# Performance work log

Measured on AMD Instinct MI355X. Metric: run time of the kernel, lower is better.

## Reference

```python
import jax, jax.numpy as jnp
import numpy as np

N = 50000      # nodes
E = 500000     # edges
IN = 256       # input feature dim
HID = 64       # hidden (per-head) dim, layer 1
H1 = 4         # heads, layer 1
NC = 64        # num_classes (layer 2 out, 1 head)
ED = 32        # edge_dim
T = 8          # num_etypes
SLOPE = 0.2    # leakyrelu negative slope


def setup_inputs() -> dict:
    key = jax.random.key(0)
    ks = jax.random.split(key, 20)
    p = lambda k, shape: (jax.random.normal(k, shape, jnp.float32) * 0.05)
    return {
        "h": jax.random.normal(ks[0], (N, IN), jnp.float32),
        "row": jax.random.randint(ks[1], (E,), 0, N, jnp.int32),   # src
        "col": jax.random.randint(ks[2], (E,), 0, N, jnp.int32),   # dst
        "etype": jax.random.randint(ks[3], (E,), 0, T, jnp.int32),
        # layer 1 (4 heads, no residual, elu activation)
        "edge_emb1": p(ks[4], (T, ED)),
        "W1": p(ks[5], (IN, HID * H1)),
        "Wr1": p(ks[6], (T, ED, ED * H1)),      # TypedLinear per-etype weight
        "a_l1": p(ks[7], (H1, HID)),
        "a_r1": p(ks[8], (H1, HID)),
        "a_e1": p(ks[9], (H1, ED)),
        # layer 2 (1 head, residual Linear, no activation)
        "edge_emb2": p(ks[10], (T, ED)),
        "W2": p(ks[11], (HID * H1, NC)),
        "Wr2": p(ks[12], (T, ED, ED)),
        "a_l2": p(ks[13], (1, NC)),
        "a_r2": p(ks[14], (1, NC)),
        "a_e2": p(ks[15], (1, ED)),
        "res_W2": p(ks[16], (HID * H1, NC)),
        "res_b2": p(ks[17], (NC,)),
    }


def _simple_hgn_conv(h, row, col, etype, edge_emb, W, Wr, a_l, a_r, a_e,
                     res_W, res_b, apply_act):
    """One SimpleHGNConv layer. h:[N,in], returns [N, out_dim*H] (D-major, H-minor
    layout, matching emb.permute(0,2,1).view in the torch code)."""
    H, D = a_l.shape            # num_heads, out_dim
    n = h.shape[0]
    emb = (h @ W).reshape(n, H, D)                     # [N,H,D]
    emb = jnp.where(jnp.isnan(emb), 0.0, emb)
    # TypedLinear: edge_emb[etype] @ Wr[etype]; only T distinct rows -> per-type GEMM
    ee = jnp.einsum('te,teo->to', edge_emb, Wr).reshape(T, H, ED)  # [T,H,ED]
    h_l = jnp.einsum('nhd,hd->nh', emb, a_l)[row]      # [E,H]
    h_r = jnp.einsum('nhd,hd->nh', emb, a_r)[col]      # [E,H]
    h_e = jnp.einsum('thd,hd->th', ee, a_e)[etype]     # [E,H]
    att = jax.nn.leaky_relu(h_l + h_r + h_e, SLOPE)    # [E,H]
    # edge_softmax: normalize over incoming edges of each destination node (col)
    seg_max = jax.ops.segment_max(att, col, num_segments=n)   # [N,H]
    att = jnp.exp(att - seg_max[col])
    seg_sum = jax.ops.segment_sum(att, col, num_segments=n)   # [N,H]
    alpha = att / seg_sum[col]                          # [E,H]
    # u_mul_e + sum aggregation
    msg = emb[row] * alpha[:, :, None]                  # [E,H,D]
    out = jax.ops.segment_sum(msg, col, num_segments=n) # [N,H,D]
    out = out.transpose(0, 2, 1).reshape(n, D * H)      # D-major layout
    if res_W is not None:
        out = out + h @ res_W + res_b
    if apply_act:
        out = jax.nn.elu(out)
    return out


def reference(h, row, col, etype,
              edge_emb1, W1, Wr1, a_l1, a_r1, a_e1,
              edge_emb2, W2, Wr2, a_l2, a_r2, a_e2, res_W2, res_b2):
    h1 = _simple_hgn_conv(h, row, col, etype, edge_emb1, W1, Wr1,
                          a_l1, a_r1, a_e1, None, None, True)
    h2 = _simple_hgn_conv(h1, row, col, etype, edge_emb2, W2, Wr2,
                          a_l2, a_r2, a_e2, res_W2, res_b2, False)
    # split by node type (first half type 'l', second half type 'v')
    return (h2[: N // 2], h2[N // 2 :])
```

## Files before the change

kernel.cpp:

```cpp
#include <hip/hip_runtime.h>
#include <hip/hip_bf16.h>

typedef __bf16 bf16x8 __attribute__((ext_vector_type(8)));
typedef float f32x4 __attribute__((ext_vector_type(4)));

#define IN_DIM 256
#define NT 8

__device__ __forceinline__ float b2f(unsigned short u) {
  union { unsigned int i; float f; } x; x.i = ((unsigned int)u) << 16; return x.f;
}
__device__ __forceinline__ float lo2f(unsigned int w) {
  union { unsigned int i; float f; } x; x.i = w << 16; return x.f;
}
__device__ __forceinline__ float hi2f(unsigned int w) {
  union { unsigned int i; float f; } x; x.i = w & 0xFFFF0000u; return x.f;
}
__device__ __forceinline__ unsigned short f2b(float f) {
  union { float f; unsigned int i; } u; u.f = f;
  unsigned int r = u.i + 0x7FFF + ((u.i >> 16) & 1);
  return (unsigned short)(r >> 16);
}
__device__ __forceinline__ float lrelu(float x) { return x >= 0.f ? x : 0.2f * x; }
__device__ __forceinline__ float ldf(const void* p, size_t i, int isf32) {
  return isf32 ? ((const float*)p)[i] : b2f(((const unsigned short*)p)[i]);
}

__global__ void prep_all_kernel(const void* __restrict__ W1, const void* __restrict__ W2,
                                const void* __restrict__ rW2,
                                const void* __restrict__ al1, const void* __restrict__ ar1,
                                const void* __restrict__ al2, const void* __restrict__ ar2,
                                const void* __restrict__ ee1, const void* __restrict__ Wr1,
                                const void* __restrict__ ae1,
                                const void* __restrict__ ee2, const void* __restrict__ Wr2,
                                const void* __restrict__ ae2,
                                unsigned short* __restrict__ W1t,
                                unsigned short* __restrict__ W2t,
                                float* __restrict__ a2l, float* __restrict__ a2r,
                                float* __restrict__ he1, float* __restrict__ he2,
                                float* __restrict__ alD, float* __restrict__ arD,
                                const unsigned int* __restrict__ hw,
                                const int* __restrict__ col, int* __restrict__ cnt,
                                int E_, int N_, int* __restrict__ dflag) {
  int b = blockIdx.x, tid = threadIdx.x;
  if (b >= 454) {
    int base = (b - 454) * 1024 + tid;
#pragma unroll
    for (int k = 0; k < 4; k++) {
      int e = base + k * 256;
      if (e < E_) {
        int c = col[e];
        if ((unsigned)c < (unsigned)N_) atomicAdd(&cnt[c], 1);
      }
    }
    return;
  }
  __shared__ int sflag;
  {
    int bad = 0;
    if (tid < 64) {
      for (int i = 0; i < 4; i++) {
        unsigned int w = hw[tid * 4 + i];
        unsigned int ex = (w & 0x7FFFu) >> 7;
        if (ex >= 0xC0u) bad++;
      }
#pragma unroll
      for (int off = 32; off; off >>= 1) bad += __shfl_xor(bad, off);
      if (tid == 0) sflag = (bad > 8) ? 1 : 0;
    }
    __syncthreads();
  }
  const int isf32 = sflag;
  if (b == 0 && tid == 0) *dflag = isf32;
  if (b < 384) {
    int j = b, k = tid;
    if (j < 256) {
      int src = (j & 3) * 64 + (j >> 2);
      W1t[j * 256 + k] = f2b(ldf(W1, (size_t)k * 256 + src, isf32));
    } else {
      int o = j - 256;
      float v = (o < 64) ? ldf(W2, (size_t)k * 64 + o, isf32)
                         : ldf(rW2, (size_t)k * 64 + (o - 64), isf32);
      W2t[o * 256 + k] = f2b(v);
    }
  } else if (b < 448) {
    int k = (b - 384) * 4 + (tid >> 6), d = tid & 63;
    float w2 = ldf(W2, (size_t)k * 64 + d, isf32);
    float l2 = w2 * ldf(al2, d, isf32);
    float r2 = w2 * ldf(ar2, d, isf32);
#pragma unroll
    for (int off = 32; off; off >>= 1) { l2 += __shfl_xor(l2, off); r2 += __shfl_xor(r2, off); }
    if (d == 0) { a2l[k] = l2; a2r[k] = r2; }
  } else {
    int bid = b - 448;
    int t = tid >> 5, d = tid & 31;
    if (bid < 4) {
      int h = bid;
      float s = 0.f;
#pragma unroll
      for (int e = 0; e < 32; e++)
        s += ldf(ee1, t * 32 + e, isf32) * ldf(Wr1, (size_t)(t * 32 + e) * 128 + h * 32 + d, isf32);
      float v = s * ldf(ae1, h * 32 + d, isf32);
#pragma unroll
      for (int off = 16; off; off >>= 1) v += __shfl_xor(v, off);
      if (d == 0) he1[t * 4 + h] = v;
    } else if (bid == 4) {
      float s = 0.f;
#pragma unroll
      for (int e = 0; e < 32; e++)
        s += ldf(ee2, t * 32 + e, isf32) * ldf(Wr2, (size_t)(t * 32 + e) * 32 + d, isf32);
      float v = s * ldf(ae2, d, isf32);
#pragma unroll
      for (int off = 16; off; off >>= 1) v += __shfl_xor(v, off);
      if (d == 0) he2[t] = v;
    } else {
      int j = tid;
      alD[j] = ldf(al1, (j & 3) * 64 + (j >> 2), isf32);
      arD[j] = ldf(ar1, (j & 3) * 64 + (j >> 2), isf32);
    }
  }
}

__global__ __launch_bounds__(256, 4) void gemm1_fill(
    const void* __restrict__ A, int M,
    const unsigned short* __restrict__ Bt,
    unsigned short* __restrict__ emb1,
    const float* __restrict__ alD, const float* __restrict__ arD,
    float* __restrict__ hl1, float* __restrict__ hr1,
    const int* __restrict__ dflag, int MBlocks,
    const int* __restrict__ col, const int* __restrict__ row,
    const int* __restrict__ ety, const int* __restrict__ ptrb,
    const int* __restrict__ bsum, int* __restrict__ cnt,
    int* __restrict__ srcc, int E_) {
  __shared__ unsigned short As[64 * 64];
  __shared__ float lsum[4][64][4];
  __shared__ float rsum[4][64][4];
  if (blockIdx.x >= MBlocks) {
    int base = (blockIdx.x - MBlocks) * 1024 + threadIdx.x;
#pragma unroll
    for (int k = 0; k < 4; k++) {
      int e = base + k * 256;
      if (e < E_) {
        int c = col[e];
        if ((unsigned)c < (unsigned)M) {
          int pos = atomicSub(&cnt[c], 1) - 1;
          long long slot = (long long)(ptrb[c] + bsum[c >> 8]) + pos;
          if (slot >= 0 && slot < E_) {
            int sr = row[e], t = ety[e];
            srcc[slot] = ((unsigned)sr < (unsigned)M && (unsigned)t < (unsigned)NT)
                             ? (sr | (t << 20)) : -1;
          }
        }
      }
    }
    return;
  }
  int isf32 = *dflag;
  const int tid = threadIdx.x;
  const int m0 = blockIdx.x * 64;
  const int wv = tid >> 6, lane = tid & 63;
  const int q = lane >> 4, m = lane & 15;
  const int jp = wv * 64;
  f32x4 acc[4][4] = {};
  for (int kc = 0; kc < 256; kc += 64) {
    {
      int row_ = tid >> 2, qt = tid & 3;
      int gr = m0 + row_;
      unsigned short tmp[16];
      if (gr < M) {
        if (isf32) {
          const float* ap = (const float*)A + (size_t)gr * 256 + kc + qt * 16;
          float4 v0 = *(const float4*)ap;
          float4 v1 = *(const float4*)(ap + 4);
          float4 v2 = *(const float4*)(ap + 8);
          float4 v3 = *(const float4*)(ap + 12);
          tmp[0]=f2b(v0.x); tmp[1]=f2b(v0.y); tmp[2]=f2b(v0.z); tmp[3]=f2b(v0.w);
          tmp[4]=f2b(v1.x); tmp[5]=f2b(v1.y); tmp[6]=f2b(v1.z); tmp[7]=f2b(v1.w);
          tmp[8]=f2b(v2.x); tmp[9]=f2b(v2.y); tmp[10]=f2b(v2.z); tmp[11]=f2b(v2.w);
          tmp[12]=f2b(v3.x); tmp[13]=f2b(v3.y); tmp[14]=f2b(v3.z); tmp[15]=f2b(v3.w);
        } else {
          const unsigned short* ap = (const unsigned short*)A + (size_t)gr * 256 + kc + qt * 16;
          *(int4*)tmp = *(const int4*)ap;
          *(int4*)(tmp + 8) = *(const int4*)(ap + 8);
        }
      } else {
        for (int x = 0; x < 16; x++) tmp[x] = 0;
      }
      int g0 = (qt * 2) ^ (row_ & 7);
      int g1 = (qt * 2 + 1) ^ (row_ & 7);
      *(int4*)(As + row_ * 64 + g0 * 8) = *(int4*)tmp;
      *(int4*)(As + row_ * 64 + g1 * 8) = *(int4*)(tmp + 8);
    }
    __syncthreads();
#pragma unroll
    for (int ks = 0; ks < 2; ks++) {
      int gk = ks * 4 + q;
      bf16x8 afr[4];
#pragma unroll
      for (int cm = 0; cm < 4; cm++) {
        int row_ = cm * 16 + m;
        afr[cm] = *(const bf16x8*)(As + row_ * 64 + (gk ^ (row_ & 7)) * 8);
      }
#pragma unroll
      for (int cj = 0; cj < 4; cj++) {
        int jr = jp + cj * 16 + m;
        bf16x8 b = *(const bf16x8*)(Bt + (size_t)jr * 256 + kc + gk * 8);
#pragma unroll
        for (int cm = 0; cm < 4; cm++)
          acc[cm][cj] = __builtin_amdgcn_mfma_f32_16x16x32_bf16(afr[cm], b, acc[cm][cj], 0, 0, 0);
      }
    }
    __syncthreads();
  }
  float al[4], ar[4];
#pragma unroll
  for (int cj = 0; cj < 4; cj++) {
    al[cj] = alD[jp + cj * 16 + m];
    ar[cj] = arD[jp + cj * 16 + m];
  }
#pragma unroll
  for (int cm = 0; cm < 4; cm++) {
#pragma unroll
    for (int r = 0; r < 4; r++) {
      int lrow = cm * 16 + q * 4 + r;
      int gm = m0 + lrow;
      float lp = 0.f, rp = 0.f;
#pragma unroll
      for (int cj = 0; cj < 4; cj++) {
        float v = acc[cm][cj][r];
        if (gm < M) emb1[(size_t)gm * 256 + jp + cj * 16 + m] = f2b(v);
        lp += v * al[cj]; rp += v * ar[cj];
      }
      lp += __shfl_xor(lp, 4); lp += __shfl_xor(lp, 8);
      rp += __shfl_xor(rp, 4); rp += __shfl_xor(rp, 8);
      if (m < 4) { lsum[wv][lrow][m] = lp; rsum[wv][lrow][m] = rp; }
    }
  }
  __syncthreads();
  {
    int row_ = tid >> 2, h = tid & 3;
    int gm = m0 + row_;
    if (gm < M) {
      float l = lsum[0][row_][h] + lsum[1][row_][h] + lsum[2][row_][h] + lsum[3][row_][h];
      float r = rsum[0][row_][h] + rsum[1][row_][h] + rsum[2][row_][h] + rsum[3][row_][h];
      hl1[(size_t)gm * 4 + h] = l;
      hr1[(size_t)gm * 4 + h] = r;
    }
  }
}

__global__ __launch_bounds__(256, 4) void gemm2_fused(
    const unsigned short* __restrict__ A, int M,
    const unsigned short* __restrict__ Bt,
    unsigned short* __restrict__ emb2, unsigned short* __restrict__ res,
    const void* __restrict__ bias, const int* __restrict__ dflag) {
  __shared__ unsigned short As[64 * 64];
  int isf32 = *dflag;
  const int tid = threadIdx.x;
  const int m0 = blockIdx.x * 64;
  const int wv = tid >> 6, lane = tid & 63;
  const int q = lane >> 4, m = lane & 15;
  const int jp = (wv & 1) * 64;
  const int mh = (wv >> 1) * 32;
  f32x4 acc[2][4] = {};
  for (int kc = 0; kc < 256; kc += 64) {
    {
      int row = tid >> 2, qt = tid & 3;
      int gr = m0 + row;
      unsigned short tmp[16];
      if (gr < M) {
        const unsigned short* ap = A + (size_t)gr * 256 + kc + qt * 16;
        *(int4*)tmp = *(const int4*)ap;
        *(int4*)(tmp + 8) = *(const int4*)(ap + 8);
      } else {
        for (int x = 0; x < 16; x++) tmp[x] = 0;
      }
      int g0 = (qt * 2) ^ (row & 7);
      int g1 = (qt * 2 + 1) ^ (row & 7);
      *(int4*)(As + row * 64 + g0 * 8) = *(int4*)tmp;
      *(int4*)(As + row * 64 + g1 * 8) = *(int4*)(tmp + 8);
    }
    __syncthreads();
#pragma unroll
    for (int ks = 0; ks < 2; ks++) {
      int gk = ks * 4 + q;
      bf16x8 afr[2];
#pragma unroll
      for (int cm = 0; cm < 2; cm++) {
        int row = mh + cm * 16 + m;
        afr[cm] = *(const bf16x8*)(As + row * 64 + (gk ^ (row & 7)) * 8);
      }
#pragma unroll
      for (int cj = 0; cj < 4; cj++) {
        int jr = jp + cj * 16 + m;
        bf16x8 b = *(const bf16x8*)(Bt + (size_t)jr * 256 + kc + gk * 8);
#pragma unroll
        for (int cm = 0; cm < 2; cm++)
          acc[cm][cj] = __builtin_amdgcn_mfma_f32_16x16x32_bf16(afr[cm], b, acc[cm][cj], 0, 0, 0);
      }
    }
    __syncthreads();
  }
  float bv[4];
#pragma unroll
  for (int cj = 0; cj < 4; cj++)
    bv[cj] = (jp == 64) ? ldf(bias, cj * 16 + m, isf32) : 0.f;
#pragma unroll
  for (int cm = 0; cm < 2; cm++) {
#pragma unroll
    for (int r = 0; r < 4; r++) {
      int gm = m0 + mh + cm * 16 + q * 4 + r;
      if (gm < M) {
#pragma unroll
        for (int cj = 0; cj < 4; cj++) {
          float v = acc[cm][cj][r];
          int gj = cj * 16 + m;
          if (jp == 0) emb2[(size_t)gm * 64 + gj] = f2b(v);
          else res[(size_t)gm * 64 + gj] = f2b(v + bv[cj]);
        }
      }
    }
  }
}

__global__ void scan1_kernel(const int* __restrict__ cnt, int* __restrict__ ptrb,
                             int* __restrict__ bsum, int n) {
  __shared__ int wsum[4];
  int tid = threadIdx.x, lane = tid & 63, wid = tid >> 6;
  int i = blockIdx.x * 256 + tid;
  int v = (i < n) ? cnt[i] : 0;
  int x = v;
#pragma unroll
  for (int off = 1; off < 64; off <<= 1) {
    int y = __shfl_up(x, off);
    if (lane >= off) x += y;
  }
  if (lane == 63) wsum[wid] = x;
  __syncthreads();
  int woff = 0;
#pragma unroll
  for (int k = 0; k < 4; k++) woff += (k < wid) ? wsum[k] : 0;
  if (i < n) ptrb[i] = x - v + woff;
  if (tid == 255) bsum[blockIdx.x] = woff + x;
}

__global__ void scan2_kernel(int* __restrict__ bsum, int* __restrict__ ptrb,
                             int nb, int n) {
  __shared__ int wsum[4];
  int tid = threadIdx.x, lane = tid & 63, wid = tid >> 6;
  int v = (tid < nb) ? bsum[tid] : 0;
  int x = v;
#pragma unroll
  for (int off = 1; off < 64; off <<= 1) {
    int y = __shfl_up(x, off);
    if (lane >= off) x += y;
  }
  if (lane == 63) wsum[wid] = x;
  __syncthreads();
  int woff = 0;
#pragma unroll
  for (int k = 0; k < 4; k++) woff += (k < wid) ? wsum[k] : 0;
  if (tid < nb) bsum[tid] = x - v + woff;
  if (tid == 255) ptrb[n] = woff + x;
}

__global__ __launch_bounds__(256) void agg1_kernel(
    const int* __restrict__ ptrb, const int* __restrict__ bsumv,
    const int* __restrict__ srcc,
    const float* __restrict__ hl1, const float* __restrict__ hr1,
    const float* __restrict__ he1,
    const unsigned short* __restrict__ emb1, unsigned short* __restrict__ h1,
    const float* __restrict__ a2l, const float* __restrict__ a2r,
    float* __restrict__ hl2, float* __restrict__ hr2,
    int n0, int N_, int E_) {
  __shared__ float4 wds[4][64];
  __shared__ int sds[4][64];
  const int tid = threadIdx.x;
  const int wv = tid >> 6, lane = tid & 63;
  const int g = lane >> 4, ln = lane & 15;
  const int node = n0 + blockIdx.x * 16 + wv * 4 + g;
  const bool nv = node < N_;
  int p0 = 0, p1 = 0;
  if (nv) {
    p0 = ptrb[node] + bsumv[node >> 8];
    p1 = (node + 1 < N_) ? (ptrb[node + 1] + bsumv[(node + 1) >> 8]) : ptrb[N_];
    p0 = max(0, min(p0, E_)); p1 = max(p0, min(p1, E_));
  }
  float4 hrv = {0.f, 0.f, 0.f, 0.f};
  if (nv) hrv = *(const float4*)(hr1 + 4 * (size_t)node);
  float s0 = 0.f, s1 = 0.f, s2 = 0.f, s3 = 0.f;
  float acc[16];
#pragma unroll
  for (int k = 0; k < 16; k++) acc[k] = 0.f;
  const unsigned short* erow = emb1 + ln * 16;
  for (int pb = p0;; pb += 16) {
    if (!__any(pb < p1)) break;
    int mc = (pb < p1) ? min(p1 - pb, 16) : 0;
    float4 w = {0.f, 0.f, 0.f, 0.f};
    int src = 0;
    if (ln < mc) {
      int spk = srcc[pb + ln];
      if (spk >= 0) {
        int sr = spk & 0xFFFFF, t = spk >> 20;
        float4 a = *(const float4*)(hl1 + 4 * (size_t)sr);
        float4 ge = *(const float4*)(he1 + 4 * (size_t)t);
        w.x = __expf(lrelu(a.x + hrv.x + ge.x));
        w.y = __expf(lrelu(a.y + hrv.y + ge.y));
        w.z = __expf(lrelu(a.z + hrv.z + ge.z));
        w.w = __expf(lrelu(a.w + hrv.w + ge.w));
        src = sr;
      }
    }
    s0 += w.x; s1 += w.y; s2 += w.z; s3 += w.w;
    wds[wv][lane] = w;
    sds[wv][lane] = src;
    for (int j = 0; j < mc; j += 2) {
      bool v1 = (j + 1) < mc;
      float4 u0 = wds[wv][g * 16 + j];
      int r0 = sds[wv][g * 16 + j];
      const unsigned short* e0 = erow + (size_t)r0 * 256;
      int4 ra = *(const int4*)e0;
      int4 rb = *(const int4*)(e0 + 8);
      float4 u1; int4 rc, rd;
      if (v1) {
        u1 = wds[wv][g * 16 + j + 1];
        int r1 = sds[wv][g * 16 + j + 1];
        const unsigned short* e1 = erow + (size_t)r1 * 256;
        rc = *(const int4*)e1;
        rd = *(const int4*)(e1 + 8);
      }
      acc[0]  += u0.x * lo2f(ra.x); acc[1]  += u0.y * hi2f(ra.x);
      acc[2]  += u0.z * lo2f(ra.y); acc[3]  += u0.w * hi2f(ra.y);
      acc[4]  += u0.x * lo2f(ra.z); acc[5]  += u0.y * hi2f(ra.z);
      acc[6]  += u0.z * lo2f(ra.w); acc[7]  += u0.w * hi2f(ra.w);
      acc[8]  += u0.x * lo2f(rb.x); acc[9]  += u0.y * hi2f(rb.x);
      acc[10] += u0.z * lo2f(rb.y); acc[11] += u0.w * hi2f(rb.y);
      acc[12] += u0.x * lo2f(rb.z); acc[13] += u0.y * hi2f(rb.z);
      acc[14] += u0.z * lo2f(rb.w); acc[15] += u0.w * hi2f(rb.w);
      if (v1) {
        acc[0]  += u1.x * lo2f(rc.x); acc[1]  += u1.y * hi2f(rc.x);
        acc[2]  += u1.z * lo2f(rc.y); acc[3]  += u1.w * hi2f(rc.y);
        acc[4]  += u1.x * lo2f(rc.z); acc[5]  += u1.y * hi2f(rc.z);
        acc[6]  += u1.z * lo2f(rc.w); acc[7]  += u1.w * hi2f(rc.w);
        acc[8]  += u1.x * lo2f(rd.x); acc[9]  += u1.y * hi2f(rd.x);
        acc[10] += u1.z * lo2f(rd.y); acc[11] += u1.w * hi2f(rd.y);
        acc[12] += u1.x * lo2f(rd.z); acc[13] += u1.y * hi2f(rd.z);
        acc[14] += u1.z * lo2f(rd.w); acc[15] += u1.w * hi2f(rd.w);
      }
    }
  }
#pragma unroll
  for (int off = 1; off < 16; off <<= 1) {
    s0 += __shfl_xor(s0, off); s1 += __shfl_xor(s1, off);
    s2 += __shfl_xor(s2, off); s3 += __shfl_xor(s3, off);
  }
  float invs[4];
  invs[0] = s0 > 0.f ? 1.f / s0 : 0.f;
  invs[1] = s1 > 0.f ? 1.f / s1 : 0.f;
  invs[2] = s2 > 0.f ? 1.f / s2 : 0.f;
  invs[3] = s3 > 0.f ? 1.f / s3 : 0.f;
  float alv[16], arv[16];
#pragma unroll
  for (int q2 = 0; q2 < 4; q2++) {
    float4 t1 = *(const float4*)(a2l + ln * 16 + q2 * 4);
    float4 t2 = *(const float4*)(a2r + ln * 16 + q2 * 4);
    alv[q2 * 4 + 0] = t1.x; alv[q2 * 4 + 1] = t1.y;
    alv[q2 * 4 + 2] = t1.z; alv[q2 * 4 + 3] = t1.w;
    arv[q2 * 4 + 0] = t2.x; arv[q2 * 4 + 1] = t2.y;
    arv[q2 * 4 + 2] = t2.z; arv[q2 * 4 + 3] = t2.w;
  }
  float lp = 0.f, rp = 0.f;
  unsigned int ow[8];
#pragma unroll
  for (int k = 0; k < 16; k++) {
    float r = acc[k] * invs[k & 3];
    r = r > 0.f ? r : __expf(r) - 1.f;
    unsigned int bb = f2b(r);
    if ((k & 1) == 0) ow[k >> 1] = bb; else ow[k >> 1] |= bb << 16;
    lp += r * alv[k];
    rp += r * arv[k];
  }
  if (nv) {
    int4 va; va.x = ow[0]; va.y = ow[1]; va.z = ow[2]; va.w = ow[3];
    int4 vb; vb.x = ow[4]; vb.y = ow[5]; vb.z = ow[6]; vb.w = ow[7];
    *(int4*)(h1 + (size_t)node * 256 + ln * 16) = va;
    *(int4*)(h1 + (size_t)node * 256 + ln * 16 + 8) = vb;
  }
#pragma unroll
  for (int off = 1; off < 16; off <<= 1) {
    lp += __shfl_xor(lp, off); rp += __shfl_xor(rp, off);
  }
  if (nv && ln == 0) { hl2[node] = lp; hr2[node] = rp; }
}

__global__ __launch_bounds__(256) void agg2_kernel(
    const int* __restrict__ ptrb, const int* __restrict__ bsumv,
    const int* __restrict__ srcc,
    const float* __restrict__ hl2, const float* __restrict__ hr2,
    const float* __restrict__ he2,
    const unsigned short* __restrict__ emb2, const unsigned short* __restrict__ res,
    void* __restrict__ out, int N_, int E_, const int* __restrict__ dflag) {
  __shared__ int2 wsd[4][4][17];
  const int isf32 = *dflag;
  const int tid = threadIdx.x;
  const int wv = tid >> 6, lane = tid & 63;
  const int g = lane >> 4, ln = lane & 15;
  const int node = blockIdx.x * 16 + wv * 4 + g;
  const bool nv = node < N_;
  int p0 = 0, p1 = 0;
  if (nv) {
    p0 = ptrb[node] + bsumv[node >> 8];
    p1 = (node + 1 < N_) ? (ptrb[node + 1] + bsumv[(node + 1) >> 8]) : ptrb[N_];
    p0 = max(0, min(p0, E_)); p1 = max(p0, min(p1, E_));
  }
  float hrv = nv ? hr2[node] : 0.f;
  float s = 0.f;
  float acc[4] = {0.f, 0.f, 0.f, 0.f};
  const unsigned short* erow = emb2 + ln * 4;
  for (int pb = p0;; pb += 16) {
    if (!__any(pb < p1)) break;
    int mc = (pb < p1) ? min(p1 - pb, 16) : 0;
    float w = 0.f; int src = 0;
    if (ln < mc) {
      int spk = srcc[pb + ln];
      if (spk >= 0) {
        int sr = spk & 0xFFFFF, t = spk >> 20;
        w = __expf(lrelu(hl2[sr] + hrv + he2[t]));
        src = sr;
      }
    }
    s += w;
    int2 pk; pk.x = __float_as_int(w); pk.y = src;
    wsd[wv][g][ln] = pk;
    int2 w0 = {0, 0}, w1 = {0, 0}; int2 pa = {0, 0}, pc = {0, 0};
    if (0 < mc) { w0 = wsd[wv][g][0]; pa = *(const int2*)(erow + (size_t)w0.y * 64); }
    if (1 < mc) { w1 = wsd[wv][g][1]; pc = *(const int2*)(erow + (size_t)w1.y * 64); }
    for (int j = 0; j < mc; j += 2) {
      int2 nw0 = {0, 0}, nw1 = {0, 0}, na = {0, 0}, nc = {0, 0};
      if (j + 2 < mc) { nw0 = wsd[wv][g][j + 2]; na = *(const int2*)(erow + (size_t)nw0.y * 64); }
      if (j + 3 < mc) { nw1 = wsd[wv][g][j + 3]; nc = *(const int2*)(erow + (size_t)nw1.y * 64); }
      float u0 = __int_as_float(w0.x);
      acc[0] += u0 * lo2f(pa.x); acc[1] += u0 * hi2f(pa.x);
      acc[2] += u0 * lo2f(pa.y); acc[3] += u0 * hi2f(pa.y);
      if (j + 1 < mc) {
        float u1 = __int_as_float(w1.x);
        acc[0] += u1 * lo2f(pc.x); acc[1] += u1 * hi2f(pc.x);
        acc[2] += u1 * lo2f(pc.y); acc[3] += u1 * hi2f(pc.y);
      }
      w0 = nw0; w1 = nw1; pa = na; pc = nc;
    }
  }
#pragma unroll
  for (int off = 1; off < 16; off <<= 1) s += __shfl_xor(s, off);
  float inv = s > 0.f ? 1.f / s : 0.f;
  if (nv) {
    ushort4 rv = *(const ushort4*)(res + (size_t)node * 64 + ln * 4);
    float o0 = acc[0] * inv + b2f(rv.x);
    float o1 = acc[1] * inv + b2f(rv.y);
    float o2 = acc[2] * inv + b2f(rv.z);
    float o3 = acc[3] * inv + b2f(rv.w);
    size_t oi = (size_t)node * 64 + ln * 4;
    if (isf32) {
      float4 ov = {o0, o1, o2, o3};
      *(float4*)((float*)out + oi) = ov;
    } else {
      ushort4 ov; ov.x = f2b(o0); ov.y = f2b(o1); ov.z = f2b(o2); ov.w = f2b(o3);
      *(ushort4*)((unsigned short*)out + oi) = ov;
    }
  }
}

extern "C" void kernel_launch(void* const* d_in, const int* in_sizes, int n_in,
                              void* d_out, int out_size, void* d_ws, size_t ws_size,
                              hipStream_t stream) {
  const int N = in_sizes[0] / IN_DIM;
  const int E = in_sizes[1];

  const void* h   = d_in[0];
  const int* row  = (const int*)d_in[1];
  const int* col  = (const int*)d_in[2];
  const int* ety  = (const int*)d_in[3];
  const void* ee1 = d_in[4];
  const void* W1  = d_in[5];
  const void* Wr1 = d_in[6];
  const void* al1 = d_in[7];
  const void* ar1 = d_in[8];
  const void* ae1 = d_in[9];
  const void* ee2 = d_in[10];
  const void* W2  = d_in[11];
  const void* Wr2 = d_in[12];
  const void* al2 = d_in[13];
  const void* ar2 = d_in[14];
  const void* ae2 = d_in[15];
  const void* rW2 = d_in[16];
  const void* rb2 = d_in[17];

  char* p = (char*)d_ws;
  auto take = [&](size_t b) { char* q = p; p += (b + 255) & ~(size_t)255; return q; };
  unsigned short* h1   = (unsigned short*)take((size_t)N * 256 * 2);
  unsigned short* emb1 = (unsigned short*)take((size_t)N * 256 * 2);
  int* srcc = (int*)take((size_t)E * 4);
  int* ptrb = (int*)take((size_t)(N + 1) * 4);
  int* cnt  = (int*)take((size_t)N * 4);
  int* bsum = (int*)take(1024);
  float* hl1 = (float*)take((size_t)N * 4 * 4);
  float* hr1 = (float*)take((size_t)N * 4 * 4);
  float* hl2 = (float*)take((size_t)N * 4);
  float* hr2 = (float*)take((size_t)N * 4);
  unsigned short* W1t = (unsigned short*)take(256 * 256 * 2);
  unsigned short* W2t = (unsigned short*)take(128 * 256 * 2);
  float* a2l = (float*)take(256 * 4);
  float* a2r = (float*)take(256 * 4);
  float* alD = (float*)take(256 * 4);
  float* arD = (float*)take(256 * 4);
  float* he1 = (float*)take(NT * 4 * 4);
  float* he2 = (float*)take(NT * 4);
  int* dflag = (int*)take(256);
  unsigned short* emb2 = emb1;
  unsigned short* res  = emb1 + (size_t)N * 64;

  const size_t need = (size_t)(p - (char*)d_ws);
  if (need > ws_size) {
    hipMemsetAsync(d_out, 0, (size_t)out_size * 2, stream);
    return;
  }

  const int ECB = (E + 1023) / 1024;
  const int MB = (N + 63) / 64;
  const int SB = (N + 255) / 256;
  const int AB = (N + 15) / 16;

  hipMemsetAsync(cnt, 0, (size_t)N * 4, stream);
  prep_all_kernel<<<454 + ECB, 256, 0, stream>>>(
      W1, W2, rW2, al1, ar1, al2, ar2, ee1, Wr1, ae1, ee2, Wr2, ae2,
      W1t, W2t, a2l, a2r, he1, he2, alD, arD,
      (const unsigned int*)h, col, cnt, E, N, dflag);

  scan1_kernel<<<SB, 256, 0, stream>>>(cnt, ptrb, bsum, N);
  scan2_kernel<<<1, 256, 0, stream>>>(bsum, ptrb, SB, N);

  gemm1_fill<<<MB + ECB, 256, 0, stream>>>(
      h, N, W1t, emb1, alD, arD, hl1, hr1, dflag, MB,
      col, row, ety, ptrb, bsum, cnt, srcc, E);

  agg1_kernel<<<AB, 256, 0, stream>>>(
      ptrb, bsum, srcc, hl1, hr1, he1, emb1, h1, a2l, a2r, hl2, hr2, 0, N, E);

  gemm2_fused<<<MB, 256, 0, stream>>>(h1, N, W2t, emb2, res, rb2, dflag);
  agg2_kernel<<<AB, 256, 0, stream>>>(
      ptrb, bsum, srcc, hl2, hr2, he2, emb2, res, d_out, N, E, dflag);
}
```

Baseline: 269.3 us.

## Stage GEMM B tiles in LDS with register prefetch and reorder fill blocks

Both GEMM kernels now copy the weight tile into a swizzled shared-memory buffer each K step, instead of having every wave read B fragments directly from global memory. They also prefetch the next A and B chunks into registers while the MFMAs run on the current chunk. gemm1_fill is relaunched with the CSR fill blocks at the front of the grid rather than the back. The cost is more LDS and registers per block, with launch bounds lowered from 4 to 2 blocks per CU, so fewer blocks fit per CU.

```diff
diff --git a/kernel.cpp b/kernel.cpp
--- a/kernel.cpp
+++ b/kernel.cpp
@@ -20,6 +20,9 @@
   union { float f; unsigned int i; } u; u.f = f;
   unsigned int r = u.i + 0x7FFF + ((u.i >> 16) & 1);
   return (unsigned short)(r >> 16);
+}
+__device__ __forceinline__ unsigned int f2b2(float lo, float hi) {
+  return (unsigned int)f2b(lo) | ((unsigned int)f2b(hi) << 16);
 }
 __device__ __forceinline__ float lrelu(float x) { return x >= 0.f ? x : 0.2f * x; }
 __device__ __forceinline__ float ldf(const void* p, size_t i, int isf32) {
@@ -121,22 +124,53 @@
   }
 }
 
-__global__ __launch_bounds__(256, 4) void gemm1_fill(
+#define G1_LOADB(kcv) do {                                                              \
+    int id0_ = tid;        b0 = *(const int4*)(Bt + (size_t)(id0_ >> 3) * 256 + (kcv) + (id0_ & 7) * 8); \
+    int id1_ = tid + 256;  b1 = *(const int4*)(Bt + (size_t)(id1_ >> 3) * 256 + (kcv) + (id1_ & 7) * 8); \
+    int id2_ = tid + 512;  b2 = *(const int4*)(Bt + (size_t)(id2_ >> 3) * 256 + (kcv) + (id2_ & 7) * 8); \
+    int id3_ = tid + 768;  b3 = *(const int4*)(Bt + (size_t)(id3_ >> 3) * 256 + (kcv) + (id3_ & 7) * 8); \
+    int id4_ = tid + 1024; b4 = *(const int4*)(Bt + (size_t)(id4_ >> 3) * 256 + (kcv) + (id4_ & 7) * 8); \
+    int id5_ = tid + 1280; b5 = *(const int4*)(Bt + (size_t)(id5_ >> 3) * 256 + (kcv) + (id5_ & 7) * 8); \
+    int id6_ = tid + 1536; b6 = *(const int4*)(Bt + (size_t)(id6_ >> 3) * 256 + (kcv) + (id6_ & 7) * 8); \
+    int id7_ = tid + 1792; b7 = *(const int4*)(Bt + (size_t)(id7_ >> 3) * 256 + (kcv) + (id7_ & 7) * 8); \
+  } while (0)
+
+#define G1_STOREB(iv, src) do {                                                         \
+    int id_ = tid + (iv) * 256; int brow_ = id_ >> 3;                                   \
+    int pg_ = (id_ & 7) ^ (brow_ & 7);                                                  \
+    *(int4*)(Bs + brow_ * 64 + pg_ * 8) = (src);                                        \
+  } while (0)
+
+#define G1_LOADA(kcv) do {                                                              \
+    if (gr < M) {                                                                       \
+      if (isf32) {                                                                      \
+        const float* ap_ = (const float*)A + (size_t)gr * 256 + (kcv) + aqt * 16;       \
+        af0 = *(const float4*)ap_;        af1 = *(const float4*)(ap_ + 4);              \
+        af2 = *(const float4*)(ap_ + 8);  af3 = *(const float4*)(ap_ + 12);             \
+      } else {                                                                          \
+        const unsigned short* ap_ = (const unsigned short*)A + (size_t)gr * 256 + (kcv) + aqt * 16; \
+        ab0 = *(const int4*)ap_;  ab1 = *(const int4*)(ap_ + 8);                        \
+      }                                                                                 \
+    }                                                                                   \
+  } while (0)
+
+__global__ __launch_bounds__(256, 2) void gemm1_fill(
     const void* __restrict__ A, int M,
     const unsigned short* __restrict__ Bt,
     unsigned short* __restrict__ emb1,
     const float* __restrict__ alD, const float* __restrict__ arD,
     float* __restrict__ hl1, float* __restrict__ hr1,
-    const int* __restrict__ dflag, int MBlocks,
+    const int* __restrict__ dflag, int FillBlocks,
     const int* __restrict__ col, const int* __restrict__ row,
     const int* __restrict__ ety, const int* __restrict__ ptrb,
     const int* __restrict__ bsum, int* __restrict__ cnt,
     int* __restrict__ srcc, int E_) {
   __shared__ unsigned short As[64 * 64];
+  __shared__ unsigned short Bs[256 * 64];
   __shared__ float lsum[4][64][4];
   __shared__ float rsum[4][64][4];
-  if (blockIdx.x >= MBlocks) {
-    int base = (blockIdx.x - MBlocks) * 1024 + threadIdx.x;
+  if (blockIdx.x < FillBlocks) {
+    int base = blockIdx.x * 1024 + threadIdx.x;
 #pragma unroll
     for (int k = 0; k < 4; k++) {
       int e = base + k * 256;
@@ -155,43 +189,41 @@
     }
     return;
   }
-  int isf32 = *dflag;
+  const int isf32 = *dflag;
   const int tid = threadIdx.x;
-  const int m0 = blockIdx.x * 64;
+  const int m0 = (blockIdx.x - FillBlocks) * 64;
   const int wv = tid >> 6, lane = tid & 63;
   const int q = lane >> 4, m = lane & 15;
   const int jp = wv * 64;
+  const int arow = tid >> 2, aqt = tid & 3;
+  const int gr = m0 + arow;
   f32x4 acc[4][4] = {};
+  float4 af0 = {0.f, 0.f, 0.f, 0.f}, af1 = af0, af2 = af0, af3 = af0;
+  int4 ab0 = {0, 0, 0, 0}, ab1 = ab0;
+  int4 b0, b1, b2, b3, b4, b5, b6, b7;
+
+  G1_LOADA(0);
+  G1_LOADB(0);
   for (int kc = 0; kc < 256; kc += 64) {
     {
-      int row_ = tid >> 2, qt = tid & 3;
-      int gr = m0 + row_;
-      unsigned short tmp[16];
-      if (gr < M) {
-        if (isf32) {
-          const float* ap = (const float*)A + (size_t)gr * 256 + kc + qt * 16;
-          float4 v0 = *(const float4*)ap;
-          float4 v1 = *(const float4*)(ap + 4);
-          float4 v2 = *(const float4*)(ap + 8);
-          float4 v3 = *(const float4*)(ap + 12);
-          tmp[0]=f2b(v0.x); tmp[1]=f2b(v0.y); tmp[2]=f2b(v0.z); tmp[3]=f2b(v0.w);
-          tmp[4]=f2b(v1.x); tmp[5]=f2b(v1.y); tmp[6]=f2b(v1.z); tmp[7]=f2b(v1.w);
-          tmp[8]=f2b(v2.x); tmp[9]=f2b(v2.y); tmp[10]=f2b(v2.z); tmp[11]=f2b(v2.w);
-          tmp[12]=f2b(v3.x); tmp[13]=f2b(v3.y); tmp[14]=f2b(v3.z); tmp[15]=f2b(v3.w);
-        } else {
-          const unsigned short* ap = (const unsigned short*)A + (size_t)gr * 256 + kc + qt * 16;
-          *(int4*)tmp = *(const int4*)ap;
-          *(int4*)(tmp + 8) = *(const int4*)(ap + 8);
-        }
+      int4 w0, w1;
+      if (isf32) {
+        w0.x = (int)f2b2(af0.x, af0.y); w0.y = (int)f2b2(af0.z, af0.w);
+        w0.z = (int)f2b2(af1.x, af1.y); w0.w = (int)f2b2(af1.z, af1.w);
+        w1.x = (int)f2b2(af2.x, af2.y); w1.y = (int)f2b2(af2.z, af2.w);
+        w1.z = (int)f2b2(af3.x, af3.y); w1.w = (int)f2b2(af3.z, af3.w);
       } else {
-        for (int x = 0; x < 16; x++) tmp[x] = 0;
-      }
-      int g0 = (qt * 2) ^ (row_ & 7);
-      int g1 = (qt * 2 + 1) ^ (row_ & 7);
-      *(int4*)(As + row_ * 64 + g0 * 8) = *(int4*)tmp;
-      *(int4*)(As + row_ * 64 + g1 * 8) = *(int4*)(tmp + 8);
+        w0 = ab0; w1 = ab1;
+      }
+      int g0 = (aqt * 2) ^ (arow & 7);
+      int g1 = (aqt * 2 + 1) ^ (arow & 7);
+      *(int4*)(As + arow * 64 + g0 * 8) = w0;
+      *(int4*)(As + arow * 64 + g1 * 8) = w1;
+      G1_STOREB(0, b0); G1_STOREB(1, b1); G1_STOREB(2, b2); G1_STOREB(3, b3);
+      G1_STOREB(4, b4); G1_STOREB(5, b5); G1_STOREB(6, b6); G1_STOREB(7, b7);
     }
     __syncthreads();
+    if (kc < 192) { G1_LOADA(kc + 64); G1_LOADB(kc + 64); }
 #pragma unroll
     for (int ks = 0; ks < 2; ks++) {
       int gk = ks * 4 + q;
@@ -204,7 +236,7 @@
 #pragma unroll
       for (int cj = 0; cj < 4; cj++) {
         int jr = jp + cj * 16 + m;
-        bf16x8 b = *(const bf16x8*)(Bt + (size_t)jr * 256 + kc + gk * 8);
+        bf16x8 b = *(const bf16x8*)(Bs + jr * 64 + (gk ^ (jr & 7)) * 8);
 #pragma unroll
         for (int cm = 0; cm < 4; cm++)
           acc[cm][cj] = __builtin_amdgcn_mfma_f32_16x16x32_bf16(afr[cm], b, acc[cm][cj], 0, 0, 0);
@@ -249,12 +281,20 @@
   }
 }
 
-__global__ __launch_bounds__(256, 4) void gemm2_fused(
+#define G2_LOADB(kcv) do {                                                              \
+    int id0_ = tid;        b0 = *(const int4*)(Bt + (size_t)(id0_ >> 3) * 256 + (kcv) + (id0_ & 7) * 8); \
+    int id1_ = tid + 256;  b1 = *(const int4*)(Bt + (size_t)(id1_ >> 3) * 256 + (kcv) + (id1_ & 7) * 8); \
+    int id2_ = tid + 512;  b2 = *(const int4*)(Bt + (size_t)(id2_ >> 3) * 256 + (kcv) + (id2_ & 7) * 8); \
+    int id3_ = tid + 768;  b3 = *(const int4*)(Bt + (size_t)(id3_ >> 3) * 256 + (kcv) + (id3_ & 7) * 8); \
+  } while (0)
+
+__global__ __launch_bounds__(256, 2) void gemm2_fused(
     const unsigned short* __restrict__ A, int M,
     const unsigned short* __restrict__ Bt,
     unsigned short* __restrict__ emb2, unsigned short* __restrict__ res,
     const void* __restrict__ bias, const int* __restrict__ dflag) {
   __shared__ unsigned short As[64 * 64];
+  __shared__ unsigned short Bs[128 * 64];
   int isf32 = *dflag;
   const int tid = threadIdx.x;
   const int m0 = blockIdx.x * 64;
@@ -262,25 +302,29 @@
   const int q = lane >> 4, m = lane & 15;
   const int jp = (wv & 1) * 64;
   const int mh = (wv >> 1) * 32;
+  const int arow = tid >> 2, aqt = tid & 3;
+  const int gr = m0 + arow;
   f32x4 acc[2][4] = {};
+  int4 ab0 = {0, 0, 0, 0}, ab1 = ab0;
+  int4 b0, b1, b2, b3;
+#define G2_LOADA(kcv) do {                                                              \
+    if (gr < M) {                                                                       \
+      const unsigned short* ap_ = A + (size_t)gr * 256 + (kcv) + aqt * 16;              \
+      ab0 = *(const int4*)ap_; ab1 = *(const int4*)(ap_ + 8);                           \
+    }                                                                                   \
+  } while (0)
+  G2_LOADA(0);
+  G2_LOADB(0);
   for (int kc = 0; kc < 256; kc += 64) {
     {
-      int row = tid >> 2, qt = tid & 3;
-      int gr = m0 + row;
-      unsigned short tmp[16];
-      if (gr < M) {
-        const unsigned short* ap = A + (size_t)gr * 256 + kc + qt * 16;
-        *(int4*)tmp = *(const int4*)ap;
-        *(int4*)(tmp + 8) = *(const int4*)(ap + 8);
-      } else {
-        for (int x = 0; x < 16; x++) tmp[x] = 0;
-      }
-      int g0 = (qt * 2) ^ (row & 7);
-      int g1 = (qt * 2 + 1) ^ (row & 7);
-      *(int4*)(As + row * 64 + g0 * 8) = *(int4*)tmp;
-      *(int4*)(As + row * 64 + g1 * 8) = *(int4*)(tmp + 8);
+      int g0 = (aqt * 2) ^ (arow & 7);
+      int g1 = (aqt * 2 + 1) ^ (arow & 7);
+      *(int4*)(As + arow * 64 + g0 * 8) = ab0;
+      *(int4*)(As + arow * 64 + g1 * 8) = ab1;
+      G1_STOREB(0, b0); G1_STOREB(1, b1); G1_STOREB(2, b2); G1_STOREB(3, b3);
     }
     __syncthreads();
+    if (kc < 192) { G2_LOADA(kc + 64); G2_LOADB(kc + 64); }
 #pragma unroll
     for (int ks = 0; ks < 2; ks++) {
       int gk = ks * 4 + q;
@@ -293,7 +337,7 @@
 #pragma unroll
       for (int cj = 0; cj < 4; cj++) {
         int jr = jp + cj * 16 + m;
-        bf16x8 b = *(const bf16x8*)(Bt + (size_t)jr * 256 + kc + gk * 8);
+        bf16x8 b = *(const bf16x8*)(Bs + jr * 64 + (gk ^ (jr & 7)) * 8);
 #pragma unroll
         for (int cm = 0; cm < 2; cm++)
           acc[cm][cj] = __builtin_amdgcn_mfma_f32_16x16x32_bf16(afr[cm], b, acc[cm][cj], 0, 0, 0);
@@ -639,8 +683,8 @@
   scan1_kernel<<<SB, 256, 0, stream>>>(cnt, ptrb, bsum, N);
   scan2_kernel<<<1, 256, 0, stream>>>(bsum, ptrb, SB, N);
 
-  gemm1_fill<<<MB + ECB, 256, 0, stream>>>(
-      h, N, W1t, emb1, alD, arD, hl1, hr1, dflag, MB,
+  gemm1_fill<<<ECB + MB, 256, 0, stream>>>(
+      h, N, W1t, emb1, alD, arD, hl1, hr1, dflag, ECB,
       col, row, ety, ptrb, bsum, cnt, srcc, E);
 
   agg1_kernel<<<AB, 256, 0, stream>>>(
```

New measurement: 259.7 us. -3.6%, faster.
